# Kernel tuning notes

Measured on AMD Instinct MI355X. Metric: run time of the kernel, lower is better.

## Reference

```python
import jax, jax.numpy as jnp
import numpy as np

GROUP = 64       # quantization block size along in_features
SCALING = 2.0    # delta_alpha / r = 32 / 16


def setup_inputs() -> dict:
    key = jax.random.key(0)
    k1, k2, k3, k4 = jax.random.split(key, 4)
    B, S, D_IN, D_OUT = 8, 2048, 4096, 4096
    x = jax.random.normal(k1, (B, S, D_IN), dtype=jnp.float32)
    # int4 codes in [0, 16); symmetric zero-point 8
    w_codes = jax.random.randint(k2, (D_OUT, D_IN), 0, 16, dtype=jnp.int32)
    # per-(row, group) scales; small positive values like bnb absmax/7
    scales = jax.random.uniform(k3, (D_OUT, D_IN // GROUP), dtype=jnp.float32) * 0.02
    base_bias = jax.random.normal(k4, (D_OUT,), dtype=jnp.float32)
    delta_w = jax.random.normal(jax.random.fold_in(key, 5), (D_OUT, D_IN), dtype=jnp.float32) * 0.01
    return {"x": x, "w_codes": w_codes, "scales": scales,
            "base_bias": base_bias, "delta_w": delta_w}


def _dequant(w_codes, scales):
    # symmetric int4 dequant: w = (code - 8) * scale_of_its_group
    d_out, d_in = w_codes.shape
    w = (w_codes.astype(scales.dtype) - 8.0).reshape(d_out, d_in // GROUP, GROUP)
    w = w * scales[:, :, None]
    return w.reshape(d_out, d_in)


def reference(x, w_codes, scales, base_bias, delta_w):
    # base layer: int4 dequant-matmul + bias
    w = _dequant(w_codes, scales)                       # [D_out, D_in]
    base = jnp.einsum("bsi,oi->bso", x, w) + base_bias  # [B, S, D_out]
    # delta branch: dropout(p=0) -> matmul -> scale -> residual add
    delta = jnp.einsum("bsi,oi->bso", x, delta_w) * SCALING
    return base + delta
```

## Files before the change

kernel.cpp:

```cpp
#include <hip/hip_runtime.h>
#include <cstdint>

#define D_IN   4096
#define D_OUT  4096
#define MTOT   16384
#define SCALING 2.0f

#define BM 256
#define BN 256
#define BK 64
#define KT (D_IN / BK)

typedef float  f32x4  __attribute__((ext_vector_type(4)));
typedef __bf16 bf16x8 __attribute__((ext_vector_type(8)));
typedef unsigned short ushort8 __attribute__((ext_vector_type(8)));
typedef int    int4v  __attribute__((ext_vector_type(4)));
typedef float  float4v __attribute__((ext_vector_type(4)));

__device__ __forceinline__ unsigned short f2bf(float f) {
  union { float f; unsigned u; } v; v.f = f;
  unsigned r = v.u + 0x7FFF + ((v.u >> 16) & 1);
  return (unsigned short)(r >> 16);
}

#define ASYNC16(g, l)                                                        \
  __builtin_amdgcn_global_load_lds(                                          \
      (const __attribute__((address_space(1))) unsigned int*)(g),            \
      (__attribute__((address_space(3))) unsigned int*)(l), 16, 0, 0)

#define BAR    __builtin_amdgcn_s_barrier()
#define LGKM0  asm volatile("s_waitcnt lgkmcnt(0)" ::: "memory")
#define VM4    asm volatile("s_waitcnt vmcnt(4)" ::: "memory")
#define VM0    asm volatile("s_waitcnt vmcnt(0)" ::: "memory")

__global__ __launch_bounds__(256) void prep_x_kernel(const float* __restrict__ x,
                                                     unsigned short* __restrict__ xbf) {
  int i = (blockIdx.x * 256 + threadIdx.x) * 8;
  float4v lo = *(const float4v*)(x + i);
  float4v hi = *(const float4v*)(x + i + 4);
  ushort8 o;
  o[0] = f2bf(lo[0]); o[1] = f2bf(lo[1]); o[2] = f2bf(lo[2]); o[3] = f2bf(lo[3]);
  o[4] = f2bf(hi[0]); o[5] = f2bf(hi[1]); o[6] = f2bf(hi[2]); o[7] = f2bf(hi[3]);
  *(ushort8*)(xbf + i) = o;
}

__global__ __launch_bounds__(256) void prep_w_kernel(const int* __restrict__ codes,
                                                     const float* __restrict__ scales,
                                                     const float* __restrict__ delta,
                                                     unsigned short* __restrict__ weff) {
  int i = (blockIdx.x * 256 + threadIdx.x) * 8;
  int row = i >> 12;
  int col = i & (D_IN - 1);
  float s = scales[(row << 6) + (col >> 6)];
  int4v   c0 = *(const int4v*)(codes + i);
  int4v   c1 = *(const int4v*)(codes + i + 4);
  float4v d0 = *(const float4v*)(delta + i);
  float4v d1 = *(const float4v*)(delta + i + 4);
  ushort8 o;
  o[0] = f2bf((float)(c0[0] - 8) * s + SCALING * d0[0]);
  o[1] = f2bf((float)(c0[1] - 8) * s + SCALING * d0[1]);
  o[2] = f2bf((float)(c0[2] - 8) * s + SCALING * d0[2]);
  o[3] = f2bf((float)(c0[3] - 8) * s + SCALING * d0[3]);
  o[4] = f2bf((float)(c1[0] - 8) * s + SCALING * d1[0]);
  o[5] = f2bf((float)(c1[1] - 8) * s + SCALING * d1[1]);
  o[6] = f2bf((float)(c1[2] - 8) * s + SCALING * d1[2]);
  o[7] = f2bf((float)(c1[3] - 8) * s + SCALING * d1[3]);
  *(ushort8*)(weff + i) = o;
}


#define STAGE_A(buf_, kt_, h_) do {                                          \
    char* d_ = &lds[buf_][h_][0] + tid * 16;                                 \
    const unsigned short* s_ = gA + (size_t)(h_) * 128 * D_IN + (kt_) * 64;  \
    ASYNC16(s_, d_);                                                         \
    ASYNC16(s_ + 64 * D_IN, d_ + 8192);                                      \
  } while (0)

#define STAGE_B(buf_, kt_, h_) do {                                          \
    char* d_ = &lds[buf_][2 + (h_)][0] + tid * 16;                           \
    const unsigned short* s_ = gB + (size_t)(h_) * 128 * D_IN + (kt_) * 64;  \
    ASYNC16(s_, d_);                                                         \
    ASYNC16(s_ + 64 * D_IN, d_ + 8192);                                      \
  } while (0)

#define RD_A(buf_, mh_, dst_) do {                                           \
    _Pragma("unroll")                                                        \
    for (int m2 = 0; m2 < 4; ++m2) {                                         \
      const char* p_ = &lds[buf_][wr][0] + ((mh_)*4 + m2) * 2048 + rowb;     \
      dst_[m2][0] = *(const bf16x8*)(p_ + koff0);                            \
      dst_[m2][1] = *(const bf16x8*)(p_ + koff1);                            \
    } } while (0)

#define RD_B(buf_, nh_, dst_) do {                                           \
    _Pragma("unroll")                                                        \
    for (int n2 = 0; n2 < 2; ++n2) {                                         \
      const char* p_ = &lds[buf_][2 + (wc >> 1)][0] + (wc & 1) * 8192 +      \
                       (nh_) * 4096 + n2 * 2048 + rowb;                      \
      dst_[n2][0] = *(const bf16x8*)(p_ + koff0);                            \
      dst_[n2][1] = *(const bf16x8*)(p_ + koff1);                            \
    } } while (0)

#define MM(afr_, bfr_, mh_, nh_) do {                                        \
    __builtin_amdgcn_s_setprio(1);                                           \
    _Pragma("unroll")                                                        \
    for (int m2 = 0; m2 < 4; ++m2) {                                         \
      _Pragma("unroll")                                                      \
      for (int n2 = 0; n2 < 2; ++n2) {                                       \
        acc[(mh_)*4 + m2][(nh_)*2 + n2] = __builtin_amdgcn_mfma_f32_16x16x32_bf16( \
            afr_[m2][0], bfr_[n2][0], acc[(mh_)*4 + m2][(nh_)*2 + n2], 0, 0, 0);   \
        acc[(mh_)*4 + m2][(nh_)*2 + n2] = __builtin_amdgcn_mfma_f32_16x16x32_bf16( \
            afr_[m2][1], bfr_[n2][1], acc[(mh_)*4 + m2][(nh_)*2 + n2], 0, 0, 0);   \
      } }                                                                    \
    __builtin_amdgcn_s_setprio(0);                                           \
  } while (0)

__global__ __launch_bounds__(512, 2) void gemm8_kernel(const unsigned short* __restrict__ xbf,
                                                       const unsigned short* __restrict__ weff,
                                                       const float* __restrict__ bias,
                                                       float* __restrict__ out) {
  __shared__ __attribute__((aligned(1024))) char lds[2][4][16384];

  const int tid  = threadIdx.x;
  const int lane = tid & 63;
  const int wid  = tid >> 6;
  const int wr   = wid >> 2;
  const int wc   = wid & 3;

  const int id  = blockIdx.x;
  const int nid = (id & 7) * 128 + (id >> 3);
  const int tn  = nid & 15;
  const int tm  = nid >> 4;

  const int rowb  = (lane & 15) * 128;
  const int kx    = (lane & 7) << 4;
  const int koff0 = (((lane >> 4) * 16) ^ kx);
  const int koff1 = ((64 + (lane >> 4) * 16) ^ kx);

  const int sr = tid >> 3;
  const int ke = ((tid & 7) ^ (sr & 7)) * 8;
  const unsigned short* gA = xbf  + (size_t)(tm * BM + sr) * D_IN + ke;
  const unsigned short* gB = weff + (size_t)(tn * BN + sr) * D_IN + ke;

  f32x4 acc[8][4] = {};
  bf16x8 a[4][2], b0[2][2], b1[2][2];

  STAGE_A(0, 0, 0); STAGE_A(0, 0, 1);
  STAGE_B(0, 0, 0); STAGE_B(0, 0, 1);
  STAGE_B(1, 1, 0); STAGE_B(1, 1, 1);
  VM4;
  BAR;

  int buf = 0;
  for (int g = 0; g < KT; ++g) {
    RD_A(buf, 0, a); RD_B(buf, 0, b0);
    if (g + 1 < KT) STAGE_A(buf ^ 1, g + 1, 0);
    BAR; LGKM0;
    MM(a, b0, 0, 0);
    BAR;
    RD_B(buf, 1, b1);
    if (g + 1 < KT) STAGE_A(buf ^ 1, g + 1, 1);
    BAR; LGKM0;
    MM(a, b1, 0, 1);
    BAR;
    RD_A(buf, 1, a);
    if (g + 2 < KT) STAGE_B(buf, g + 2, 0);
    BAR; LGKM0;
    MM(a, b0, 1, 0);
    BAR;
    if (g + 2 < KT) STAGE_B(buf, g + 2, 1);
    BAR; LGKM0;
    MM(a, b1, 1, 1);
    if (g < KT - 2) { VM4; } else { VM0; }
    BAR;
    buf ^= 1;
  }

  const int row0 = tm * BM + wr * 128 + (lane >> 4) * 4;
  const int col0 = tn * BN + wc * 64 + (lane & 15);
#pragma unroll
  for (int n = 0; n < 4; ++n) {
    const int col = col0 + n * 16;
    const float bv = bias[col];
#pragma unroll
    for (int m = 0; m < 8; ++m) {
      const int r = row0 + m * 16;
#pragma unroll
      for (int j = 0; j < 4; ++j)
        out[(size_t)(r + j) * D_OUT + col] = acc[m][n][j] + bv;
    }
  }
}

extern "C" void kernel_launch(void* const* d_in, const int* in_sizes, int n_in,
                              void* d_out, int out_size, void* d_ws, size_t ws_size,
                              hipStream_t stream) {
  const float* x      = (const float*)d_in[0];
  const int*   codes  = (const int*)d_in[1];
  const float* scales = (const float*)d_in[2];
  const float* bias   = (const float*)d_in[3];
  const float* delta  = (const float*)d_in[4];
  float* out = (float*)d_out;

  unsigned short* xbf  = (unsigned short*)d_ws;
  unsigned short* weff = xbf + (size_t)MTOT * D_IN;

  prep_x_kernel<<<(MTOT * D_IN) / (256 * 8), 256, 0, stream>>>(x, xbf);
  prep_w_kernel<<<(D_OUT * D_IN) / (256 * 8), 256, 0, stream>>>(codes, scales, delta, weff);

  gemm8_kernel<<<(MTOT / BM) * (D_OUT / BN), 512, 0, stream>>>(xbf, weff, bias, out);
}
```

Before: 579.4 us.

## Software-pipeline LDS fragment reads across k-tiles with double A registers

```diff
diff --git a/kernel.cpp b/kernel.cpp
--- a/kernel.cpp
+++ b/kernel.cpp
@@ -28,10 +28,7 @@
       (const __attribute__((address_space(1))) unsigned int*)(g),            \
       (__attribute__((address_space(3))) unsigned int*)(l), 16, 0, 0)
 
-#define BAR    __builtin_amdgcn_s_barrier()
-#define LGKM0  asm volatile("s_waitcnt lgkmcnt(0)" ::: "memory")
-#define VM4    asm volatile("s_waitcnt vmcnt(4)" ::: "memory")
-#define VM0    asm volatile("s_waitcnt vmcnt(0)" ::: "memory")
+#define BAR __builtin_amdgcn_s_barrier()
 
 __global__ __launch_bounds__(256) void prep_x_kernel(const float* __restrict__ x,
                                                      unsigned short* __restrict__ xbf) {
@@ -114,6 +111,34 @@
     __builtin_amdgcn_s_setprio(0);                                           \
   } while (0)
 
+#define KTILE(buf_, g_, SA_, SB_, VMTOK_, PRE_) do {                         \
+                                                                     \
+    RD_B(buf_, 1, b1);                                                       \
+    if (SA_) STAGE_A(1 - (buf_), (g_) + 1, 0);                               \
+    BAR;                                                                     \
+    MM(aE, b0, 0, 0);                                                        \
+    BAR;                                                                     \
+                                                                     \
+    RD_A(buf_, 1, aO);                                                       \
+    if (SA_) STAGE_A(1 - (buf_), (g_) + 1, 1);                               \
+    BAR;                                                                     \
+    MM(aE, b1, 0, 1);                                                        \
+    BAR;                                                                     \
+                                                                     \
+    if (SB_) STAGE_B(buf_, (g_) + 2, 0);                                     \
+    asm volatile("s_waitcnt vmcnt(" VMTOK_ ")" ::: "memory");                \
+    if (PRE_) RD_A(1 - (buf_), 0, aE);                                       \
+    BAR;                                                                     \
+    MM(aO, b0, 1, 0);                                                        \
+    BAR;                                                                     \
+                                                                     \
+    if (PRE_) RD_B(1 - (buf_), 0, b0);                                       \
+    if (SB_) STAGE_B(buf_, (g_) + 2, 1);                                     \
+    BAR;                                                                     \
+    MM(aO, b1, 1, 1);                                                        \
+    BAR;                                                                     \
+  } while (0)
+
 __global__ __launch_bounds__(512, 2) void gemm8_kernel(const unsigned short* __restrict__ xbf,
                                                        const unsigned short* __restrict__ weff,
                                                        const float* __restrict__ bias,
@@ -141,52 +166,39 @@
   const unsigned short* gA = xbf  + (size_t)(tm * BM + sr) * D_IN + ke;
   const unsigned short* gB = weff + (size_t)(tn * BN + sr) * D_IN + ke;
 
+  const int col0 = tn * BN + wc * 64 + (lane & 15);
+
   f32x4 acc[8][4] = {};
-  bf16x8 a[4][2], b0[2][2], b1[2][2];
+  bf16x8 aE[4][2], aO[4][2], b0[2][2], b1[2][2];
+
+  float bv[4];
+#pragma unroll
+  for (int n = 0; n < 4; ++n) bv[n] = bias[col0 + n * 16];
 
   STAGE_A(0, 0, 0); STAGE_A(0, 0, 1);
   STAGE_B(0, 0, 0); STAGE_B(0, 0, 1);
   STAGE_B(1, 1, 0); STAGE_B(1, 1, 1);
-  VM4;
+  asm volatile("s_waitcnt vmcnt(4)" ::: "memory");
   BAR;
-
-  int buf = 0;
-  for (int g = 0; g < KT; ++g) {
-    RD_A(buf, 0, a); RD_B(buf, 0, b0);
-    if (g + 1 < KT) STAGE_A(buf ^ 1, g + 1, 0);
-    BAR; LGKM0;
-    MM(a, b0, 0, 0);
-    BAR;
-    RD_B(buf, 1, b1);
-    if (g + 1 < KT) STAGE_A(buf ^ 1, g + 1, 1);
-    BAR; LGKM0;
-    MM(a, b1, 0, 1);
-    BAR;
-    RD_A(buf, 1, a);
-    if (g + 2 < KT) STAGE_B(buf, g + 2, 0);
-    BAR; LGKM0;
-    MM(a, b0, 1, 0);
-    BAR;
-    if (g + 2 < KT) STAGE_B(buf, g + 2, 1);
-    BAR; LGKM0;
-    MM(a, b1, 1, 1);
-    if (g < KT - 2) { VM4; } else { VM0; }
-    BAR;
-    buf ^= 1;
+  RD_A(0, 0, aE); RD_B(0, 0, b0);
+
+  for (int g = 0; g < KT - 2; g += 2) {
+    KTILE(0, g,     1, 1, "2", 1);
+    KTILE(1, g + 1, 1, 1, "2", 1);
   }
+  KTILE(0, KT - 2, 1, 0, "0", 1);
+  KTILE(1, KT - 1, 0, 0, "0", 0);
 
   const int row0 = tm * BM + wr * 128 + (lane >> 4) * 4;
-  const int col0 = tn * BN + wc * 64 + (lane & 15);
 #pragma unroll
   for (int n = 0; n < 4; ++n) {
     const int col = col0 + n * 16;
-    const float bv = bias[col];
 #pragma unroll
     for (int m = 0; m < 8; ++m) {
       const int r = row0 + m * 16;
 #pragma unroll
       for (int j = 0; j < 4; ++j)
-        out[(size_t)(r + j) * D_OUT + col] = acc[m][n][j] + bv;
+        out[(size_t)(r + j) * D_OUT + col] = acc[m][n][j] + bv[n];
     }
   }
 }
```

New measurement: 695.5 us. 20.0% more time.
